# Kernel optimization log

Hardware: AMD Instinct MI355X
Metric: run time of the kernel (lower is better)

## Reference

```python
import jax, jax.numpy as jnp
import numpy as np

N_NODES = 100000
N_EDGES = 1600000
IN_DIM = 256
HIDDEN = 128
N_CLASSES = 40


def gcn_conv(x, W, b, src, dst, n_nodes):
    """torch_geometric GCNConv: transform -> add self-loops -> sym-normalized sum-aggregate -> +bias."""
    h = x @ W  # [N, out]
    loop = jnp.arange(n_nodes, dtype=src.dtype)
    src2 = jnp.concatenate([src, loop])
    dst2 = jnp.concatenate([dst, loop])
    # degree with self-loops (edge weight 1)
    deg = jax.ops.segment_sum(jnp.ones_like(dst2, dtype=h.dtype), dst2, num_segments=n_nodes)
    dinv = jnp.where(deg > 0, jax.lax.rsqrt(deg), 0.0)
    norm = dinv[src2] * dinv[dst2]  # [E+N]
    msg = h[src2] * norm[:, None]   # [E+N, out] gather + scale
    out = jax.ops.segment_sum(msg, dst2, num_segments=n_nodes)
    return out + b


def setup_inputs() -> dict:
    key = jax.random.key(0)
    k1, k2, k3, k4 = jax.random.split(key, 4)
    x = jax.random.normal(k1, (N_NODES, IN_DIM), dtype=jnp.float32)
    edge_index = jax.random.randint(k2, (2, N_EDGES), 0, N_NODES, dtype=jnp.int64)
    W1 = jax.random.normal(k3, (IN_DIM, HIDDEN), dtype=jnp.float32) * (1.0 / np.sqrt(IN_DIM))
    b1 = jnp.zeros((HIDDEN,), dtype=jnp.float32)
    W2 = jax.random.normal(k4, (HIDDEN, N_CLASSES), dtype=jnp.float32) * (1.0 / np.sqrt(HIDDEN))
    b2 = jnp.zeros((N_CLASSES,), dtype=jnp.float32)
    return {"x": x, "edge_index": edge_index, "W1": W1, "b1": b1, "W2": W2, "b2": b2}


def reference(x, edge_index, W1, b1, W2, b2):
    src, dst = edge_index[0], edge_index[1]
    h = gcn_conv(x, W1, b1, src, dst, N_NODES)
    h = jax.nn.relu(h)
    # dropout p=0.5 is identity in eval mode
    out = gcn_conv(h, W2, b2, src, dst, N_NODES)
    return out
```

## Files before the change

### kernel.cpp

```cpp
#include <hip/hip_runtime.h>
#include <hip/hip_bf16.h>
#include <hip/hip_fp16.h>

#define N_NODES 100000
#define N_EDGES 1600000
#define IN_DIM 256
#define HIDDEN 128
#define NCLS 40
#define NCLS_PAD 48

#define N_BUCKETS 256
#define NPB 391
#define BCAP 8192
#define EPT 16
#define BIN_WG 4096
#define BIN_BLOCKS 391

typedef __attribute__((ext_vector_type(8))) _Float16 half8;
typedef __attribute__((ext_vector_type(4))) float floatx4;


__global__ __launch_bounds__(256) void k_bin(const int* __restrict__ src, const int* __restrict__ dst,
                                             int* __restrict__ bfill,
                                             int* __restrict__ bsrc, int* __restrict__ bdst,
                                             const float* __restrict__ W1, __half* __restrict__ W1T,
                                             const float* __restrict__ W2, __half* __restrict__ W2T) {
    const int t = threadIdx.x;
    if (blockIdx.x >= BIN_BLOCKS) {
        int wb = blockIdx.x - BIN_BLOCKS;
        if (wb < 128) {
            int i = wb * 256 + t;
            int k = i >> 7, n = i & 127;
            W1T[n * IN_DIM + k] = __float2half_rn(W1[i]);
        } else {
            for (int i = t; i < NCLS_PAD * HIDDEN; i += 256) {
                int n = i >> 7, k = i & 127;
                W2T[n * HIDDEN + k] = (n < NCLS) ? __float2half_rn(W2[k * NCLS + n]) : __float2half_rn(0.f);
            }
        }
        return;
    }
    __shared__ int hist[N_BUCKETS];
    __shared__ int base[N_BUCKETS];
    hist[t] = 0;
    __syncthreads();
    const long e0 = (long)blockIdx.x * BIN_WG;
    int msrc[EPT], mdst[EPT], moff[EPT];
    #pragma unroll
    for (int i = 0; i < EPT; i++) {
        long e = e0 + t + i * 256;
        if (e < N_EDGES) {
            msrc[i] = src[e];
            mdst[i] = dst[e];
            moff[i] = atomicAdd(&hist[mdst[i] / NPB], 1);
        } else {
            mdst[i] = -1;
        }
    }
    __syncthreads();
    int h = hist[t];
    base[t] = (h > 0) ? atomicAdd(&bfill[t], h) : 0;
    __syncthreads();
    #pragma unroll
    for (int i = 0; i < EPT; i++) {
        if (mdst[i] >= 0) {
            int b = mdst[i] / NPB;
            int p = base[b] + moff[i];
            bsrc[b * BCAP + p] = msrc[i];
            bdst[b * BCAP + p] = mdst[i];
        }
    }
}


__global__ __launch_bounds__(256) void k_build(const int* __restrict__ bfill,
                                               const int* __restrict__ bsrc, const int* __restrict__ bdst,
                                               int* __restrict__ row_ptr, float* __restrict__ dinv,
                                               int* __restrict__ col) {
    __shared__ int h[NPB];
    __shared__ int pfx[NPB];
    __shared__ int sred[4];
    const int b  = blockIdx.x;
    const int nb = b * NPB;
    const int nn = min(NPB, N_NODES - nb);
    const int t  = threadIdx.x;
    int v = (t < b) ? bfill[t] : 0;
    #pragma unroll
    for (int dl = 32; dl > 0; dl >>= 1) v += __shfl_down(v, dl, 64);
    if ((t & 63) == 0) sred[t >> 6] = v;
    for (int i = t; i < NPB; i += 256) h[i] = 0;
    __syncthreads();
    const int base_b = sred[0] + sred[1] + sred[2] + sred[3];
    const int n = bfill[b];
    for (int i = t; i < n; i += 256) atomicAdd(&h[bdst[b * BCAP + i] - nb], 1);
    __syncthreads();
    if (t < 64) {
        int carry = 0;
        #pragma unroll
        for (int c = 0; c < (NPB + 63) / 64; c++) {
            int idx = c * 64 + t;
            int hv = (idx < nn) ? h[idx] : 0;
            int s = hv;
            #pragma unroll
            for (int d2 = 1; d2 < 64; d2 <<= 1) {
                int u = __shfl_up(s, d2, 64);
                if (t >= d2) s += u;
            }
            if (idx < nn) {
                int ex = base_b + carry + (s - hv);
                pfx[idx] = ex;
                row_ptr[nb + idx] = ex;
                dinv[nb + idx] = rsqrtf((float)(hv + 1));
            }
            carry += __shfl(s, 63, 64);
        }
    }
    __syncthreads();
    for (int i = t; i < nn; i += 256) h[i] = 0;
    __syncthreads();
    for (int i = t; i < n; i += 256) {
        int dd = bdst[b * BCAP + i];
        int ss = bsrc[b * BCAP + i];
        int pos = pfx[dd - nb] + atomicAdd(&h[dd - nb], 1);
        col[pos] = ss;
    }
    if (b == 0 && t == 0) row_ptr[N_NODES] = N_EDGES;
}


__global__ __launch_bounds__(256) void k_gemm1(const float* __restrict__ X,
                                               const __half* __restrict__ W1T,
                                               const float* __restrict__ dinv,
                                               __half* __restrict__ H1s) {
    __shared__ __align__(16) _Float16 Asm[128][72];
    __shared__ __align__(16) _Float16 Bsm[128][72];
    const int tid  = threadIdx.x;
    const int wave = tid >> 6;
    const int lane = tid & 63;
    const int m16  = lane & 15;
    const int kq   = lane >> 4;
    const int row0 = blockIdx.x * 128;

    floatx4 acc[2][8];
    #pragma unroll
    for (int mt = 0; mt < 2; mt++)
        #pragma unroll
        for (int i = 0; i < 8; i++) acc[mt][i] = (floatx4)0.f;

    for (int kc = 0; kc < 4; kc++) {
        #pragma unroll
        for (int it = 0; it < 4; it++) {
            int u = tid + it * 256;
            int r = u >> 3, j = u & 7;
            int gr = row0 + r;
            float4 x0 = make_float4(0.f, 0.f, 0.f, 0.f), x1 = x0;
            if (gr < N_NODES) {
                const float* p = &X[(long)gr * IN_DIM + kc * 64 + j * 8];
                x0 = *(const float4*)p;
                x1 = *(const float4*)(p + 4);
            }
            half8 h;
            h[0] = (_Float16)x0.x; h[1] = (_Float16)x0.y; h[2] = (_Float16)x0.z; h[3] = (_Float16)x0.w;
            h[4] = (_Float16)x1.x; h[5] = (_Float16)x1.y; h[6] = (_Float16)x1.z; h[7] = (_Float16)x1.w;
            *(half8*)&Asm[r][j * 8] = h;
        }
        #pragma unroll
        for (int it = 0; it < 4; it++) {
            int u = tid + it * 256;
            int n = u >> 3, j = u & 7;
            float4 w = *(const float4*)&W1T[n * IN_DIM + kc * 64 + j * 8];
            *(float4*)&Bsm[n][j * 8] = w;
        }
        __syncthreads();
        #pragma unroll
        for (int ks = 0; ks < 2; ks++) {
            half8 a0 = *(const half8*)&Asm[wave * 32 + m16][ks * 32 + kq * 8];
            half8 a1 = *(const half8*)&Asm[wave * 32 + 16 + m16][ks * 32 + kq * 8];
            #pragma unroll
            for (int nt = 0; nt < 8; nt++) {
                half8 b = *(const half8*)&Bsm[nt * 16 + m16][ks * 32 + kq * 8];
                acc[0][nt] = __builtin_amdgcn_mfma_f32_16x16x32_f16(a0, b, acc[0][nt], 0, 0, 0);
                acc[1][nt] = __builtin_amdgcn_mfma_f32_16x16x32_f16(a1, b, acc[1][nt], 0, 0, 0);
            }
        }
        __syncthreads();
    }
    #pragma unroll
    for (int mt = 0; mt < 2; mt++) {
        const int gr0 = row0 + wave * 32 + mt * 16 + kq * 4;
        float dd[4];
        #pragma unroll
        for (int r = 0; r < 4; r++) dd[r] = (gr0 + r < N_NODES) ? dinv[gr0 + r] : 0.f;
        #pragma unroll
        for (int nt = 0; nt < 8; nt++) {
            int c = nt * 16 + m16;
            #pragma unroll
            for (int r = 0; r < 4; r++) {
                if (gr0 + r < N_NODES)
                    H1s[(long)(gr0 + r) * HIDDEN + c] = __float2half_rn(dd[r] * acc[mt][nt][r]);
            }
        }
    }
}


__global__ __launch_bounds__(256) void k_agg1(const __half* __restrict__ H1s,
                                              const int* __restrict__ row_ptr,
                                              const int* __restrict__ col,
                                              const float* __restrict__ dinv,
                                              const float* __restrict__ b1,
                                              __half* __restrict__ H1a) {
    int d = blockIdx.x * 4 + (threadIdx.x >> 6);
    int lane = threadIdx.x & 63;
    int e0 = row_ptr[d], e1 = row_ptr[d + 1];
    const __half2* base = (const __half2*)H1s;
    float ax = 0.f, ay = 0.f;
    int e = e0;
    for (; e + 3 < e1; e += 4) {
        int s0 = col[e], s1 = col[e + 1], s2 = col[e + 2], s3 = col[e + 3];
        float2 f0 = __half22float2(base[(long)s0 * 64 + lane]);
        float2 f1 = __half22float2(base[(long)s1 * 64 + lane]);
        float2 f2 = __half22float2(base[(long)s2 * 64 + lane]);
        float2 f3 = __half22float2(base[(long)s3 * 64 + lane]);
        ax += f0.x + f1.x + f2.x + f3.x;
        ay += f0.y + f1.y + f2.y + f3.y;
    }
    for (; e < e1; e++) {
        float2 f = __half22float2(base[(long)col[e] * 64 + lane]);
        ax += f.x; ay += f.y;
    }
    float2 fs = __half22float2(base[(long)d * 64 + lane]);
    ax += fs.x; ay += fs.y;
    float dd = dinv[d];
    float2 bb = ((const float2*)b1)[lane];
    float ox = fmaxf(dd * ax + bb.x, 0.f);
    float oy = fmaxf(dd * ay + bb.y, 0.f);
    ((__half2*)H1a)[(long)d * 64 + lane] = __halves2half2(__float2half_rn(ox), __float2half_rn(oy));
}


__global__ __launch_bounds__(256) void k_gemm2(const __half* __restrict__ H1a,
                                               const __half* __restrict__ W2T,
                                               const float* __restrict__ dinv,
                                               __half* __restrict__ H2s) {
    const int wave = threadIdx.x >> 6;
    const int lane = threadIdx.x & 63;
    const int m16  = lane & 15;
    const int kq   = lane >> 4;
    const int rowa = min(blockIdx.x * 64 + wave * 16 + m16, N_NODES - 1);

    floatx4 acc[3];
    #pragma unroll
    for (int i = 0; i < 3; i++) acc[i] = (floatx4)0.f;

    #pragma unroll
    for (int ks = 0; ks < 4; ks++) {
        half8 a = *(const half8*)&H1a[(long)rowa * HIDDEN + ks * 32 + kq * 8];
        #pragma unroll
        for (int nt = 0; nt < 3; nt++) {
            half8 b = *(const half8*)&W2T[(nt * 16 + m16) * HIDDEN + ks * 32 + kq * 8];
            acc[nt] = __builtin_amdgcn_mfma_f32_16x16x32_f16(a, b, acc[nt], 0, 0, 0);
        }
    }
    const int gr0 = blockIdx.x * 64 + wave * 16 + kq * 4;
    float dd[4];
    #pragma unroll
    for (int r = 0; r < 4; r++) dd[r] = (gr0 + r < N_NODES) ? dinv[gr0 + r] : 0.f;
    #pragma unroll
    for (int nt = 0; nt < 3; nt++) {
        int c = nt * 16 + m16;
        if (c < NCLS) {
            #pragma unroll
            for (int r = 0; r < 4; r++) {
                if (gr0 + r < N_NODES)
                    H2s[(long)(gr0 + r) * NCLS + c] = __float2half_rn(dd[r] * acc[nt][r]);
            }
        }
    }
}


__global__ __launch_bounds__(256) void k_agg2(const __half* __restrict__ H2s,
                                              const int* __restrict__ row_ptr,
                                              const int* __restrict__ col,
                                              const float* __restrict__ dinv,
                                              const float* __restrict__ b2,
                                              float* __restrict__ out) {
    const int wave = threadIdx.x >> 6;
    const int lane = threadIdx.x & 63;
    const int g = lane / 20;
    const int f = lane - g * 20;
    const int d = blockIdx.x * 12 + wave * 3 + g;
    const bool act = (g < 3) && (d < N_NODES);
    int e0 = 0, e1 = 0;
    if (act) { e0 = row_ptr[d]; e1 = row_ptr[d + 1]; }
    const __half2* base2 = (const __half2*)H2s;
    float sx = 0.f, sy = 0.f;
    int e = e0;
    while (__any(e < e1)) {
        if (e < e1) {
            float2 v = __half22float2(base2[(long)col[e] * 20 + f]);
            sx += v.x; sy += v.y;
        }
        if (e + 1 < e1) {
            float2 v = __half22float2(base2[(long)col[e + 1] * 20 + f]);
            sx += v.x; sy += v.y;
        }
        e += 2;
    }
    if (act) {
        float2 v = __half22float2(base2[(long)d * 20 + f]);
        sx += v.x; sy += v.y;
        float dd = dinv[d];
        float2 bb = ((const float2*)b2)[f];
        ((float2*)out)[(long)d * 20 + f] = make_float2(dd * sx + bb.x, dd * sy + bb.y);
    }
}


extern "C" void kernel_launch(void* const* d_in, const int* in_sizes, int n_in,
                              void* d_out, int out_size, void* d_ws, size_t ws_size,
                              hipStream_t stream) {
    const float* x  = (const float*)d_in[0];
    const int*   ei = (const int*)d_in[1];
    const float* W1 = (const float*)d_in[2];
    const float* b1 = (const float*)d_in[3];
    const float* W2 = (const float*)d_in[4];
    const float* b2 = (const float*)d_in[5];
    const int* srcE = ei;
    const int* dstE = ei + N_EDGES;

    int*   row_ptr = (int*)d_ws;
    int*   bfill   = row_ptr + 100032;
    int*   col     = bfill + 256;
    float* dinv    = (float*)(col + N_EDGES);
    __half* H1s    = (__half*)(dinv + 100032);
    __half* H1a    = H1s + (long)N_NODES * HIDDEN;
    __half* H2s    = H1a + (long)N_NODES * HIDDEN;
    __half* W1T    = H2s + (long)N_NODES * NCLS;
    __half* W2T    = W1T + IN_DIM * HIDDEN;
    int*   bsrc    = (int*)H1s;
    int*   bdst    = bsrc + N_BUCKETS * BCAP;

    hipMemsetAsync(bfill, 0, N_BUCKETS * sizeof(int), stream);

    k_bin   <<<BIN_BLOCKS + 129, 256, 0, stream>>>(srcE, dstE, bfill, bsrc, bdst, W1, W1T, W2, W2T);
    k_build <<<N_BUCKETS, 256, 0, stream>>>(bfill, bsrc, bdst, row_ptr, dinv, col);

    k_gemm1 <<<(N_NODES + 127) / 128, 256, 0, stream>>>(x, W1T, dinv, H1s);
    k_agg1  <<<N_NODES / 4, 256, 0, stream>>>(H1s, row_ptr, col, dinv, b1, H1a);
    k_gemm2 <<<(N_NODES + 63) / 64, 256, 0, stream>>>(H1a, W2T, dinv, H2s);
    k_agg2  <<<(N_NODES + 11) / 12, 256, 0, stream>>>(H2s, row_ptr, col, dinv, b2, (float*)d_out);
}
```

Before: 404.3 us.

## Stage binned edges in LDS, pack src/dst pairs, widen agg2 loads

The edge binning kernel now sorts each block's edges by bucket in shared memory and writes packed 64-bit (dst,src) pairs contiguously per bucket, replacing scattered separate src/dst stores. The build kernel reads the packed pairs. The second aggregation kernel now handles 6 nodes per wave with 4-wide half loads and float4 stores instead of 3 nodes with half2. This targets write coalescing and fewer memory instructions, at the cost of about 45KB of shared memory per binning block, which lowers occupancy.

```diff
diff --git a/kernel.cpp b/kernel.cpp
--- a/kernel.cpp
+++ b/kernel.cpp
@@ -17,12 +17,13 @@
 #define BIN_BLOCKS 391
 
 typedef __attribute__((ext_vector_type(8))) _Float16 half8;
+typedef __attribute__((ext_vector_type(4))) _Float16 half4f;
 typedef __attribute__((ext_vector_type(4))) float floatx4;
 
 
 __global__ __launch_bounds__(256) void k_bin(const int* __restrict__ src, const int* __restrict__ dst,
                                              int* __restrict__ bfill,
-                                             int* __restrict__ bsrc, int* __restrict__ bdst,
+                                             unsigned long long* __restrict__ bpair,
                                              const float* __restrict__ W1, __half* __restrict__ W1T,
                                              const float* __restrict__ W2, __half* __restrict__ W2T) {
     const int t = threadIdx.x;
@@ -41,10 +42,14 @@
         return;
     }
     __shared__ int hist[N_BUCKETS];
-    __shared__ int base[N_BUCKETS];
+    __shared__ int bstart[N_BUCKETS];
+    __shared__ int gbase[N_BUCKETS];
+    __shared__ unsigned long long stage[BIN_WG];
+    __shared__ unsigned char bid[BIN_WG];
     hist[t] = 0;
     __syncthreads();
     const long e0 = (long)blockIdx.x * BIN_WG;
+    const int n_valid = (int)min((long)BIN_WG, (long)N_EDGES - e0);
     int msrc[EPT], mdst[EPT], moff[EPT];
     #pragma unroll
     for (int i = 0; i < EPT; i++) {
@@ -58,23 +63,45 @@
         }
     }
     __syncthreads();
+    if (t < 64) {
+        int carry = 0;
+        #pragma unroll
+        for (int c = 0; c < 4; c++) {
+            int idx = c * 64 + t;
+            int hv = hist[idx];
+            int s = hv;
+            #pragma unroll
+            for (int d2 = 1; d2 < 64; d2 <<= 1) {
+                int u = __shfl_up(s, d2, 64);
+                if (t >= d2) s += u;
+            }
+            bstart[idx] = carry + (s - hv);
+            carry += __shfl(s, 63, 64);
+        }
+    }
+    __syncthreads();
     int h = hist[t];
-    base[t] = (h > 0) ? atomicAdd(&bfill[t], h) : 0;
-    __syncthreads();
+    gbase[t] = (h > 0) ? atomicAdd(&bfill[t], h) : 0;
     #pragma unroll
     for (int i = 0; i < EPT; i++) {
         if (mdst[i] >= 0) {
             int b = mdst[i] / NPB;
-            int p = base[b] + moff[i];
-            bsrc[b * BCAP + p] = msrc[i];
-            bdst[b * BCAP + p] = mdst[i];
-        }
+            int pos = bstart[b] + moff[i];
+            stage[pos] = ((unsigned long long)(unsigned)mdst[i] << 32) | (unsigned)msrc[i];
+            bid[pos] = (unsigned char)b;
+        }
+    }
+    __syncthreads();
+    for (int i = t; i < n_valid; i += 256) {
+        int b = bid[i];
+        int dest = gbase[b] + (i - bstart[b]);
+        bpair[(long)b * BCAP + dest] = stage[i];
     }
 }
 
 
 __global__ __launch_bounds__(256) void k_build(const int* __restrict__ bfill,
-                                               const int* __restrict__ bsrc, const int* __restrict__ bdst,
+                                               const unsigned long long* __restrict__ bpair,
                                                int* __restrict__ row_ptr, float* __restrict__ dinv,
                                                int* __restrict__ col) {
     __shared__ int h[NPB];
@@ -92,7 +119,10 @@
     __syncthreads();
     const int base_b = sred[0] + sred[1] + sred[2] + sred[3];
     const int n = bfill[b];
-    for (int i = t; i < n; i += 256) atomicAdd(&h[bdst[b * BCAP + i] - nb], 1);
+    for (int i = t; i < n; i += 256) {
+        int dd = (int)(bpair[(long)b * BCAP + i] >> 32);
+        atomicAdd(&h[dd - nb], 1);
+    }
     __syncthreads();
     if (t < 64) {
         int carry = 0;
@@ -119,8 +149,9 @@
     for (int i = t; i < nn; i += 256) h[i] = 0;
     __syncthreads();
     for (int i = t; i < n; i += 256) {
-        int dd = bdst[b * BCAP + i];
-        int ss = bsrc[b * BCAP + i];
+        unsigned long long p = bpair[(long)b * BCAP + i];
+        int dd = (int)(p >> 32);
+        int ss = (int)(p & 0xFFFFFFFFu);
         int pos = pfx[dd - nb] + atomicAdd(&h[dd - nb], 1);
         col[pos] = ss;
     }
@@ -288,32 +319,33 @@
                                               float* __restrict__ out) {
     const int wave = threadIdx.x >> 6;
     const int lane = threadIdx.x & 63;
-    const int g = lane / 20;
-    const int f = lane - g * 20;
-    const int d = blockIdx.x * 12 + wave * 3 + g;
-    const bool act = (g < 3) && (d < N_NODES);
+    const int g = lane / 10;
+    const int f = lane - g * 10;
+    const int d = blockIdx.x * 24 + wave * 6 + g;
+    const bool act = (g < 6) && (d < N_NODES);
     int e0 = 0, e1 = 0;
     if (act) { e0 = row_ptr[d]; e1 = row_ptr[d + 1]; }
-    const __half2* base2 = (const __half2*)H2s;
-    float sx = 0.f, sy = 0.f;
+    const half4f* base4 = (const half4f*)H2s;
+    float s0 = 0.f, s1 = 0.f, s2 = 0.f, s3 = 0.f;
     int e = e0;
     while (__any(e < e1)) {
         if (e < e1) {
-            float2 v = __half22float2(base2[(long)col[e] * 20 + f]);
-            sx += v.x; sy += v.y;
+            half4f v = base4[(long)col[e] * 10 + f];
+            s0 += (float)v[0]; s1 += (float)v[1]; s2 += (float)v[2]; s3 += (float)v[3];
         }
         if (e + 1 < e1) {
-            float2 v = __half22float2(base2[(long)col[e + 1] * 20 + f]);
-            sx += v.x; sy += v.y;
+            half4f v = base4[(long)col[e + 1] * 10 + f];
+            s0 += (float)v[0]; s1 += (float)v[1]; s2 += (float)v[2]; s3 += (float)v[3];
         }
         e += 2;
     }
     if (act) {
-        float2 v = __half22float2(base2[(long)d * 20 + f]);
-        sx += v.x; sy += v.y;
+        half4f v = base4[(long)d * 10 + f];
+        s0 += (float)v[0]; s1 += (float)v[1]; s2 += (float)v[2]; s3 += (float)v[3];
         float dd = dinv[d];
-        float2 bb = ((const float2*)b2)[f];
-        ((float2*)out)[(long)d * 20 + f] = make_float2(dd * sx + bb.x, dd * sy + bb.y);
+        float4 bb = ((const float4*)b2)[f];
+        float4 o = make_float4(dd * s0 + bb.x, dd * s1 + bb.y, dd * s2 + bb.z, dd * s3 + bb.w);
+        ((float4*)out)[(long)d * 10 + f] = o;
     }
 }
 
@@ -339,16 +371,15 @@
     __half* H2s    = H1a + (long)N_NODES * HIDDEN;
     __half* W1T    = H2s + (long)N_NODES * NCLS;
     __half* W2T    = W1T + IN_DIM * HIDDEN;
-    int*   bsrc    = (int*)H1s;
-    int*   bdst    = bsrc + N_BUCKETS * BCAP;
+    unsigned long long* bpair = (unsigned long long*)H1s;
 
     hipMemsetAsync(bfill, 0, N_BUCKETS * sizeof(int), stream);
 
-    k_bin   <<<BIN_BLOCKS + 129, 256, 0, stream>>>(srcE, dstE, bfill, bsrc, bdst, W1, W1T, W2, W2T);
-    k_build <<<N_BUCKETS, 256, 0, stream>>>(bfill, bsrc, bdst, row_ptr, dinv, col);
+    k_bin   <<<BIN_BLOCKS + 129, 256, 0, stream>>>(srcE, dstE, bfill, bpair, W1, W1T, W2, W2T);
+    k_build <<<N_BUCKETS, 256, 0, stream>>>(bfill, bpair, row_ptr, dinv, col);
 
     k_gemm1 <<<(N_NODES + 127) / 128, 256, 0, stream>>>(x, W1T, dinv, H1s);
     k_agg1  <<<N_NODES / 4, 256, 0, stream>>>(H1s, row_ptr, col, dinv, b1, H1a);
     k_gemm2 <<<(N_NODES + 63) / 64, 256, 0, stream>>>(H1a, W2T, dinv, H2s);
-    k_agg2  <<<(N_NODES + 11) / 12, 256, 0, stream>>>(H2s, row_ptr, col, dinv, b2, (float*)d_out);
-}
+    k_agg2  <<<(N_NODES + 23) / 24, 256, 0, stream>>>(H2s, row_ptr, col, dinv, b2, (float*)d_out);
+}
```

Measured after the change: 375.1 us. -7.2%, faster.
